# Kernel optimization log

Measured on AMD Instinct MI355X. Metric: run time of the kernel, lower is better.

## Reference

```python
import jax, jax.numpy as jnp
import numpy as np

N_NODES = 50000


def _gcn_conv(x, src, dst, W, b, n_nodes):
    # x: [N, Fin] -> h: [N, Fout]; GCN: D^-1/2 (A+I) D^-1/2 (x W) + b
    h = x @ W
    deg = jax.ops.segment_sum(jnp.ones_like(dst, dtype=h.dtype), dst,
                              num_segments=n_nodes)
    dinv = jax.lax.rsqrt(jnp.maximum(deg, 1.0))
    norm = dinv[src] * dinv[dst]                      # [E]
    msg = h[src] * norm[:, None]                      # [E, Fout] gather
    agg = jax.ops.segment_sum(msg, dst, num_segments=n_nodes)  # scatter-add
    return agg + b


def setup_inputs() -> dict:
    key = jax.random.key(0)
    k0, k1, k2, k3 = jax.random.split(key, 4)
    N, E, F_IN, H, C = N_NODES, 800000, 128, 128, 16
    x = jax.random.normal(k0, (N, F_IN), dtype=jnp.float32)
    edge_index = jax.random.randint(k1, (2, E), 0, N, dtype=jnp.int64)
    W1 = jax.random.normal(k2, (F_IN, H), dtype=jnp.float32) / np.sqrt(F_IN)
    b1 = jnp.zeros((H,), dtype=jnp.float32)
    W2 = jax.random.normal(k3, (H, C), dtype=jnp.float32) / np.sqrt(H)
    b2 = jnp.zeros((C,), dtype=jnp.float32)
    return {"x": x, "edge_index": edge_index, "W1": W1, "b1": b1,
            "W2": W2, "b2": b2}


def reference(x, edge_index, W1, b1, W2, b2):
    n = x.shape[0]
    # add self-loops (shared by both conv layers)
    loops = jnp.arange(n, dtype=edge_index.dtype)
    src = jnp.concatenate([edge_index[0], loops])
    dst = jnp.concatenate([edge_index[1], loops])
    h = _gcn_conv(x, src, dst, W1, b1, n)
    h = jax.nn.relu(h)
    # dropout p=0.5 is identity in eval mode
    h = _gcn_conv(h, src, dst, W2, b2, n)
    return jax.nn.log_softmax(h, axis=1)
```

## Files before the change

kernel.cpp:

```cpp
#include <hip/hip_runtime.h>
#include <math.h>


#define NBUCKET_SHIFT 8
#define BIN_CHUNK 4096

typedef __bf16 bf16x8 __attribute__((ext_vector_type(8)));
typedef float  f32x4  __attribute__((ext_vector_type(4)));

__device__ __forceinline__ unsigned short pack_bf16(float f) {
    unsigned u = __float_as_uint(f);
    return (unsigned short)((u + 0x7fffu + ((u >> 16) & 1u)) >> 16);
}

__device__ __forceinline__ unsigned pack_bf16x2(float a, float b) {
    return ((unsigned)pack_bf16(b) << 16) | pack_bf16(a);
}

__device__ __forceinline__ float2 unpack_bf16x2(unsigned u) {
    return make_float2(__uint_as_float(u << 16), __uint_as_float(u & 0xffff0000u));
}

__device__ __forceinline__ void acc_u4(float* a, uint4 v) {
    float2 t;
    t = unpack_bf16x2(v.x); a[0] += t.x; a[1] += t.y;
    t = unpack_bf16x2(v.y); a[2] += t.x; a[3] += t.y;
    t = unpack_bf16x2(v.z); a[4] += t.x; a[5] += t.y;
    t = unpack_bf16x2(v.w); a[6] += t.x; a[7] += t.y;
}

__global__ __launch_bounds__(256)
void count_wt_kernel(const int* __restrict__ dst, int* __restrict__ bktcnt,
                     int E, int nbuckets, int nbins,
                     const float* __restrict__ W, unsigned short* __restrict__ wtp) {
    const int blk = blockIdx.x;
    const int tid = threadIdx.x;
    if (blk >= nbins) {
        int idx = (blk - nbins) * 256 + tid;
        int j    = idx & 7;
        int lane = (idx >> 3) & 63;
        int ks   = (idx >> 9) & 3;
        int t    = idx >> 11;
        int n = t * 16 + (lane & 15);
        int k = ks * 32 + ((lane >> 4) << 3) + j;
        wtp[idx] = pack_bf16(W[k * 128 + n]);
        return;
    }
    __shared__ int cnt[256];
    cnt[tid] = 0;
    __syncthreads();
    const int e0 = blk * BIN_CHUNK;
    const int n = min(BIN_CHUNK, E - e0);
    for (int i = tid; i < n; i += 256)
        atomicAdd(&cnt[dst[e0 + i] >> NBUCKET_SHIFT], 1);
    __syncthreads();
    if (tid < nbuckets && cnt[tid] > 0) atomicAdd(&bktcnt[tid], cnt[tid]);
}

__global__ __launch_bounds__(256)
void bin_kernel(const int* __restrict__ src, const int* __restrict__ dst,
                const int* __restrict__ bktcnt, int* __restrict__ bcur,
                unsigned* __restrict__ pairs, int E, int nbuckets) {
    __shared__ unsigned spair[BIN_CHUNK];
    __shared__ int lcnt[256];
    __shared__ int lbase[256];
    __shared__ int sbase[256];
    const int tid = threadIdx.x;
    const int e0 = blockIdx.x * BIN_CHUNK;
    const int cnt = min(BIN_CHUNK, E - e0);

    int v = (tid < nbuckets) ? bktcnt[tid] : 0;
    sbase[tid] = v;
    lcnt[tid] = 0;
    __syncthreads();
#pragma unroll
    for (int off = 1; off < 256; off <<= 1) {
        int u = (tid >= off) ? sbase[tid - off] : 0;
        __syncthreads();
        sbase[tid] += u;
        __syncthreads();
    }
    int excl = sbase[tid] - v;
    __syncthreads();
    sbase[tid] = excl;
    __syncthreads();

    for (int i = tid; i < cnt; i += 256) {
        unsigned s = (unsigned)src[e0 + i], d = (unsigned)dst[e0 + i];
        spair[i] = (d >> NBUCKET_SHIFT) << 24 | (d & 255u) << 16 | s;
        atomicAdd(&lcnt[d >> NBUCKET_SHIFT], 1);
    }
    __syncthreads();

    if (tid < nbuckets) {
        int c = lcnt[tid];
        lbase[tid] = (c > 0) ? atomicAdd(&bcur[tid], c) : 0;
        lcnt[tid] = 0;
    }
    __syncthreads();

    for (int i = tid; i < cnt; i += 256) {
        unsigned p = spair[i];
        int b = (int)(p >> 24);
        int off = atomicAdd(&lcnt[b], 1);
        pairs[sbase[b] + lbase[b] + off] = p;
    }
}

__global__ __launch_bounds__(256)
void bucket_build_kernel(const int* __restrict__ bktcnt, const unsigned* __restrict__ pairs,
                         int* __restrict__ rowptr, float* __restrict__ dinv,
                         int* __restrict__ colsrc, int N, int E, int nbuckets) {
    __shared__ int cnt[256];
    __shared__ int sm[256];
    const int tid = threadIdx.x;
    const int blk = blockIdx.x;
    const int nb0 = blk << NBUCKET_SHIFT;

    int bv = (tid < nbuckets) ? bktcnt[tid] : 0;
    sm[tid] = bv;
    cnt[tid] = 0;
    __syncthreads();
#pragma unroll
    for (int off = 1; off < 256; off <<= 1) {
        int u = (tid >= off) ? sm[tid - off] : 0;
        __syncthreads();
        sm[tid] += u;
        __syncthreads();
    }
    __syncthreads();
    const int hi0 = sm[blk];
    const int lo = hi0 - bktcnt[blk];
    const int hi = hi0;
    __syncthreads();

    for (int i = lo + tid; i < hi; i += 256)
        atomicAdd(&cnt[(int)(pairs[i] >> 16) & 255], 1);
    __syncthreads();

    int v = cnt[tid];
    sm[tid] = v;
    __syncthreads();
#pragma unroll
    for (int off = 1; off < 256; off <<= 1) {
        int u = (tid >= off) ? sm[tid - off] : 0;
        __syncthreads();
        sm[tid] += u;
        __syncthreads();
    }
    int excl = sm[tid] - v;
    int node = nb0 + tid;
    if (node < N) {
        rowptr[node] = lo + excl;
        dinv[node] = rsqrtf((float)v + 1.0f);
    }
    __syncthreads();
    cnt[tid] = lo + excl;
    __syncthreads();
    for (int i = lo + tid; i < hi; i += 256) {
        unsigned p = pairs[i];
        int pos = atomicAdd(&cnt[(int)(p >> 16) & 255], 1);
        colsrc[pos] = (int)(p & 0xffffu);
    }
    if (blk == 0 && tid == 0) rowptr[N] = E;
}

__global__ __launch_bounds__(256)
void gemm1_mfma_kernel(const float* __restrict__ x, const unsigned short* __restrict__ wtp,
                       const float* __restrict__ dinv, unsigned* __restrict__ h1b, int N) {
    __shared__ float lds[4][16 * 132];
    const int tid = threadIdx.x, wave = tid >> 6, lane = tid & 63;
    const int q = lane >> 4, m = lane & 15;
    const int row0 = blockIdx.x * 64 + wave * 16;
    const int row = row0 + m;
    const int rowc = (row < N) ? row : (N - 1);

    f32x4 acc[8];
#pragma unroll
    for (int t = 0; t < 8; t++) acc[t] = (f32x4)0.0f;

#pragma unroll
    for (int ks = 0; ks < 4; ks++) {
        const float4* xp = (const float4*)(x + (size_t)rowc * 128 + ks * 32 + q * 8);
        float4 f0 = xp[0], f1 = xp[1];
        float fv[8] = {f0.x, f0.y, f0.z, f0.w, f1.x, f1.y, f1.z, f1.w};
        bf16x8 ah, al;
#pragma unroll
        for (int j = 0; j < 8; j++) {
            __bf16 h = (__bf16)fv[j];
            ah[j] = h;
            al[j] = (__bf16)(fv[j] - (float)h);
        }
#pragma unroll
        for (int t = 0; t < 8; t++) {
            bf16x8 b = *(const bf16x8*)(wtp + (size_t)(t * 4 + ks) * 512 + lane * 8);
            acc[t] = __builtin_amdgcn_mfma_f32_16x16x32_bf16(ah, b, acc[t], 0, 0, 0);
            acc[t] = __builtin_amdgcn_mfma_f32_16x16x32_bf16(al, b, acc[t], 0, 0, 0);
        }
    }

#pragma unroll
    for (int t = 0; t < 8; t++)
#pragma unroll
        for (int r = 0; r < 4; r++)
            lds[wave][(q * 4 + r) * 132 + t * 16 + m] = acc[t][r];
    __syncthreads();

    const int r2 = lane >> 2, j = lane & 3;
    const int orow = row0 + r2;
    if (orow < N) {
        float dv = dinv[orow];
        const float* lrow = &lds[wave][r2 * 132];
#pragma unroll
        for (int s = 0; s < 4; s++) {
            int pp = s >> 1, ss = s & 1;
            float4 a = *(const float4*)(lrow + s * 32 + j * 8);
            float4 b = *(const float4*)(lrow + s * 32 + j * 8 + 4);
            uint4 pk;
            pk.x = pack_bf16x2(a.x * dv, a.y * dv);
            pk.y = pack_bf16x2(a.z * dv, a.w * dv);
            pk.z = pack_bf16x2(b.x * dv, b.y * dv);
            pk.w = pack_bf16x2(b.z * dv, b.w * dv);
            ((uint4*)(h1b + (size_t)pp * N * 32))[(size_t)orow * 8 + ss * 4 + j] = pk;
        }
    }
}

__global__ __launch_bounds__(256)
void l1_fused_kernel(const int* __restrict__ rowptr, const int* __restrict__ colsrc,
                     const float* __restrict__ dinv, const unsigned* __restrict__ h1b_p,
                     const float* __restrict__ b1s, const float* __restrict__ W2s,
                     float* __restrict__ h2s, int N, int accumulate) {
    __shared__ float rows[4][4][64];
    __shared__ float w2s[64 * 16];
    const int tid = threadIdx.x;
    const int wave = tid >> 6, lane = tid & 63;
    const int c = lane & 7;
    const int n = (lane >> 3) & 3;
    const int g = lane >> 5;
    const int d = blockIdx.x * 16 + wave * 4 + n;

    for (int i = tid; i < 256; i += 256)
        ((float4*)w2s)[i] = ((const float4*)W2s)[i];

    const uint4* hq = (const uint4*)h1b_p;

    if (d < N) {
        float a[8];
#pragma unroll
        for (int j = 0; j < 8; j++) a[j] = 0.0f;

        if (g == 0)
            acc_u4(a, hq[(size_t)d * 8 + c]);

        int i = rowptr[d], end = rowptr[d + 1];
        for (; i + 8 <= end; i += 8) {
            int s0 = colsrc[i + g],     s1 = colsrc[i + 2 + g];
            int s2 = colsrc[i + 4 + g], s3 = colsrc[i + 6 + g];
            uint4 v0 = hq[(size_t)s0 * 8 + c];
            uint4 v1 = hq[(size_t)s1 * 8 + c];
            uint4 v2 = hq[(size_t)s2 * 8 + c];
            uint4 v3 = hq[(size_t)s3 * 8 + c];
            acc_u4(a, v0); acc_u4(a, v1); acc_u4(a, v2); acc_u4(a, v3);
        }
        for (; i + 2 <= end; i += 2) {
            int sx = colsrc[i + g];
            acc_u4(a, hq[(size_t)sx * 8 + c]);
        }
        if (i < end && g == 0)
            acc_u4(a, hq[(size_t)colsrc[i] * 8 + c]);

#pragma unroll
        for (int j = 0; j < 8; j++)
            a[j] += __shfl_xor(a[j], 32, 64);

        if (g == 0) {
            float dv = dinv[d];
            float4 b0 = ((const float4*)b1s)[2 * c];
            float4 b1v = ((const float4*)b1s)[2 * c + 1];
            float bb[8] = {b0.x, b0.y, b0.z, b0.w, b1v.x, b1v.y, b1v.z, b1v.w};
#pragma unroll
            for (int j = 0; j < 8; j++)
                rows[wave][n][c * 8 + j] = fmaxf(a[j] * dv + bb[j], 0.0f);
        }
    }
    __syncthreads();

    const int n2 = lane >> 4, col = lane & 15;
    const int d2 = blockIdx.x * 16 + wave * 4 + n2;
    if (d2 < N) {
        const float* r = &rows[wave][n2][0];
        float p = 0.0f;
#pragma unroll
        for (int k = 0; k < 64; k++)
            p = fmaf(r[k], w2s[k * 16 + col], p);
        p *= dinv[d2];
        if (accumulate) atomicAdd(&h2s[(size_t)d2 * 16 + col], p);
        else            h2s[(size_t)d2 * 16 + col] = p;
    }
}

__global__ __launch_bounds__(256)
void l2_kernel(const int* __restrict__ rowptr, const int* __restrict__ colsrc,
               const float* __restrict__ dinv, const float* __restrict__ h2s,
               const float* __restrict__ b2, float* __restrict__ out, int N) {
    const int tid = threadIdx.x;
    const int wave = tid >> 6, lane = tid & 63;
    const int g = lane >> 2;
    const int c = lane & 3;
    const int d = blockIdx.x * 4 + wave;
    if (d >= N) return;
    const float4* h2q = (const float4*)h2s;

    float4 acc = make_float4(0.f, 0.f, 0.f, 0.f);
    if (g == 0) acc = h2q[d * 4 + c];
    int i = rowptr[d], end = rowptr[d + 1];
    for (; i + 16 <= end; i += 16) {
        int s = colsrc[i + g];
        float4 v = h2q[s * 4 + c];
        acc.x += v.x; acc.y += v.y; acc.z += v.z; acc.w += v.w;
    }
    if (i < end && g < end - i) {
        int s = colsrc[i + g];
        float4 v = h2q[s * 4 + c];
        acc.x += v.x; acc.y += v.y; acc.z += v.z; acc.w += v.w;
    }
#pragma unroll
    for (int off = 4; off <= 32; off <<= 1) {
        acc.x += __shfl_xor(acc.x, off, 64);
        acc.y += __shfl_xor(acc.y, off, 64);
        acc.z += __shfl_xor(acc.z, off, 64);
        acc.w += __shfl_xor(acc.w, off, 64);
    }
    float dv = dinv[d];
    float4 b = ((const float4*)b2)[c];
    float4 val = make_float4(acc.x * dv + b.x, acc.y * dv + b.y,
                             acc.z * dv + b.z, acc.w * dv + b.w);
    float m = fmaxf(fmaxf(val.x, val.y), fmaxf(val.z, val.w));
    m = fmaxf(m, __shfl_xor(m, 1, 64));
    m = fmaxf(m, __shfl_xor(m, 2, 64));
    float e = expf(val.x - m) + expf(val.y - m) + expf(val.z - m) + expf(val.w - m);
    e += __shfl_xor(e, 1, 64);
    e += __shfl_xor(e, 2, 64);
    float lse = m + logf(e);
    if (g == 0)
        ((float4*)out)[d * 4 + c] =
            make_float4(val.x - lse, val.y - lse, val.z - lse, val.w - lse);
}

extern "C" void kernel_launch(void* const* d_in, const int* in_sizes, int n_in,
                              void* d_out, int out_size, void* d_ws, size_t ws_size,
                              hipStream_t stream) {
    const float* x  = (const float*)d_in[0];
    const int*  ei  = (const int*)d_in[1];
    const float* W1 = (const float*)d_in[2];
    const float* b1 = (const float*)d_in[3];
    const float* W2 = (const float*)d_in[4];
    const float* b2 = (const float*)d_in[5];
    float* out = (float*)d_out;

    const int N = in_sizes[0] / 128;
    const int E = in_sizes[1] / 2;
    const int* src = ei;
    const int* dst = ei + E;
    const int nbuckets = (N + 255) >> NBUCKET_SHIFT;
    const int nbins = (E + BIN_CHUNK - 1) / BIN_CHUNK;

    float*          wsf     = (float*)d_ws;
    float*          dinv    = wsf;
    int*            rowptr  = (int*)(wsf + N);
    int*            bktcnt  = rowptr + N + 4;
    int*            bcur    = bktcnt + 256;
    unsigned short* wtp     = (unsigned short*)(bcur + 256);
    int*            colsrc  = bcur + 256 + 8192;
    unsigned*       pairs   = (unsigned*)(colsrc + E);
    unsigned*       h1b     = pairs + E;
    float*          h2s     = (float*)(h1b + (size_t)N * 64);

    hipMemsetAsync(bktcnt, 0, 512 * sizeof(int), stream);
    count_wt_kernel<<<nbins + 64, 256, 0, stream>>>(dst, bktcnt, E, nbuckets,
                                                    nbins, W1, wtp);
    bin_kernel<<<nbins, 256, 0, stream>>>(src, dst, bktcnt, bcur, pairs, E, nbuckets);
    bucket_build_kernel<<<nbuckets, 256, 0, stream>>>(bktcnt, pairs, rowptr,
                                                      dinv, colsrc, N, E, nbuckets);

    gemm1_mfma_kernel<<<(N + 63) / 64, 256, 0, stream>>>(x, wtp, dinv, h1b, N);

    {
        int blocks = (N + 15) / 16;
        for (int p = 0; p < 2; p++) {
            l1_fused_kernel<<<blocks, 256, 0, stream>>>(
                rowptr, colsrc, dinv, h1b + (size_t)p * N * 32,
                b1 + p * 64, W2 + (size_t)p * 64 * 16, h2s, N, p);
        }
    }

    l2_kernel<<<(N + 3) / 4, 256, 0, stream>>>(rowptr, colsrc, dinv, h2s, b2, out, N);
}
```

Baseline: 196.0 us.

## Merge split-feature layer-1 aggregation passes into a single full-width pass

```diff
diff --git a/kernel.cpp b/kernel.cpp
--- a/kernel.cpp
+++ b/kernel.cpp
@@ -213,7 +213,6 @@
         const float* lrow = &lds[wave][r2 * 132];
 #pragma unroll
         for (int s = 0; s < 4; s++) {
-            int pp = s >> 1, ss = s & 1;
             float4 a = *(const float4*)(lrow + s * 32 + j * 8);
             float4 b = *(const float4*)(lrow + s * 32 + j * 8 + 4);
             uint4 pk;
@@ -221,29 +220,29 @@
             pk.y = pack_bf16x2(a.z * dv, a.w * dv);
             pk.z = pack_bf16x2(b.x * dv, b.y * dv);
             pk.w = pack_bf16x2(b.z * dv, b.w * dv);
-            ((uint4*)(h1b + (size_t)pp * N * 32))[(size_t)orow * 8 + ss * 4 + j] = pk;
+            ((uint4*)h1b)[(size_t)orow * 16 + s * 4 + j] = pk;
         }
     }
 }
 
 __global__ __launch_bounds__(256)
 void l1_fused_kernel(const int* __restrict__ rowptr, const int* __restrict__ colsrc,
-                     const float* __restrict__ dinv, const unsigned* __restrict__ h1b_p,
-                     const float* __restrict__ b1s, const float* __restrict__ W2s,
-                     float* __restrict__ h2s, int N, int accumulate) {
-    __shared__ float rows[4][4][64];
-    __shared__ float w2s[64 * 16];
+                     const float* __restrict__ dinv, const unsigned* __restrict__ h1b,
+                     const float* __restrict__ b1, const float* __restrict__ W2,
+                     float* __restrict__ h2s, int N) {
+    __shared__ float rows[4][2][128];
+    __shared__ float w2s[128 * 16];
     const int tid = threadIdx.x;
     const int wave = tid >> 6, lane = tid & 63;
-    const int c = lane & 7;
-    const int n = (lane >> 3) & 3;
-    const int g = lane >> 5;
-    const int d = blockIdx.x * 16 + wave * 4 + n;
-
-    for (int i = tid; i < 256; i += 256)
-        ((float4*)w2s)[i] = ((const float4*)W2s)[i];
-
-    const uint4* hq = (const uint4*)h1b_p;
+    const int c = lane & 15;
+    const int g = (lane >> 4) & 1;
+    const int n = lane >> 5;
+    const int d = blockIdx.x * 8 + wave * 2 + n;
+
+    for (int i = tid; i < 512; i += 256)
+        ((float4*)w2s)[i] = ((const float4*)W2)[i];
+
+    const uint4* hq = (const uint4*)h1b;
 
     if (d < N) {
         float a[8];
@@ -251,33 +250,33 @@
         for (int j = 0; j < 8; j++) a[j] = 0.0f;
 
         if (g == 0)
-            acc_u4(a, hq[(size_t)d * 8 + c]);
+            acc_u4(a, hq[(size_t)d * 16 + c]);
 
         int i = rowptr[d], end = rowptr[d + 1];
         for (; i + 8 <= end; i += 8) {
             int s0 = colsrc[i + g],     s1 = colsrc[i + 2 + g];
             int s2 = colsrc[i + 4 + g], s3 = colsrc[i + 6 + g];
-            uint4 v0 = hq[(size_t)s0 * 8 + c];
-            uint4 v1 = hq[(size_t)s1 * 8 + c];
-            uint4 v2 = hq[(size_t)s2 * 8 + c];
-            uint4 v3 = hq[(size_t)s3 * 8 + c];
+            uint4 v0 = hq[(size_t)s0 * 16 + c];
+            uint4 v1 = hq[(size_t)s1 * 16 + c];
+            uint4 v2 = hq[(size_t)s2 * 16 + c];
+            uint4 v3 = hq[(size_t)s3 * 16 + c];
             acc_u4(a, v0); acc_u4(a, v1); acc_u4(a, v2); acc_u4(a, v3);
         }
         for (; i + 2 <= end; i += 2) {
             int sx = colsrc[i + g];
-            acc_u4(a, hq[(size_t)sx * 8 + c]);
+            acc_u4(a, hq[(size_t)sx * 16 + c]);
         }
         if (i < end && g == 0)
-            acc_u4(a, hq[(size_t)colsrc[i] * 8 + c]);
+            acc_u4(a, hq[(size_t)colsrc[i] * 16 + c]);
 
 #pragma unroll
         for (int j = 0; j < 8; j++)
-            a[j] += __shfl_xor(a[j], 32, 64);
+            a[j] += __shfl_xor(a[j], 16, 64);
 
         if (g == 0) {
             float dv = dinv[d];
-            float4 b0 = ((const float4*)b1s)[2 * c];
-            float4 b1v = ((const float4*)b1s)[2 * c + 1];
+            float4 b0 = ((const float4*)b1)[2 * c];
+            float4 b1v = ((const float4*)b1)[2 * c + 1];
             float bb[8] = {b0.x, b0.y, b0.z, b0.w, b1v.x, b1v.y, b1v.z, b1v.w};
 #pragma unroll
             for (int j = 0; j < 8; j++)
@@ -286,17 +285,17 @@
     }
     __syncthreads();
 
-    const int n2 = lane >> 4, col = lane & 15;
-    const int d2 = blockIdx.x * 16 + wave * 4 + n2;
+    const int n2 = lane >> 5, kh = (lane >> 4) & 1, col = lane & 15;
+    const int d2 = blockIdx.x * 8 + wave * 2 + n2;
     if (d2 < N) {
-        const float* r = &rows[wave][n2][0];
+        const float* r = &rows[wave][n2][kh * 64];
+        const float* w = &w2s[kh * 64 * 16];
         float p = 0.0f;
 #pragma unroll
         for (int k = 0; k < 64; k++)
-            p = fmaf(r[k], w2s[k * 16 + col], p);
-        p *= dinv[d2];
-        if (accumulate) atomicAdd(&h2s[(size_t)d2 * 16 + col], p);
-        else            h2s[(size_t)d2 * 16 + col] = p;
+            p = fmaf(r[k], w[k * 16 + col], p);
+        p += __shfl_xor(p, 16, 64);
+        if (kh == 0) h2s[(size_t)d2 * 16 + col] = p * dinv[d2];
     }
 }
 
@@ -386,14 +385,8 @@
 
     gemm1_mfma_kernel<<<(N + 63) / 64, 256, 0, stream>>>(x, wtp, dinv, h1b, N);
 
-    {
-        int blocks = (N + 15) / 16;
-        for (int p = 0; p < 2; p++) {
-            l1_fused_kernel<<<blocks, 256, 0, stream>>>(
-                rowptr, colsrc, dinv, h1b + (size_t)p * N * 32,
-                b1 + p * 64, W2 + (size_t)p * 64 * 16, h2s, N, p);
-        }
-    }
+    l1_fused_kernel<<<(N + 7) / 8, 256, 0, stream>>>(rowptr, colsrc, dinv, h1b,
+                                                     b1, W2, h2s, N);
 
     l2_kernel<<<(N + 3) / 4, 256, 0, stream>>>(rowptr, colsrc, dinv, h2s, b2, out, N);
 }
```

After: 195.4 us. Within noise of the previous version (-0.3%).
